# Kernel tuning notes

Measured on AMD Instinct MI355X. Metric: run time of the kernel, lower is better.

The kernel has to match this reference:

```python
import jax, jax.numpy as jnp
import numpy as np

HEADS = 16
HEAD_DIM = 64
TOKEN_DIM = 1024
INNER = HEADS * HEAD_DIM


def setup_inputs() -> dict:
    key = jax.random.key(0)
    k1, k2, k3, k4 = jax.random.split(key, 4)
    x = jax.random.normal(k1, (2, 2048, TOKEN_DIM), dtype=jnp.float32)
    # nn.Linear(token_dim, inner*3, bias=False): weight [3*inner, token_dim]
    w_qkv = jax.random.normal(k2, (3 * INNER, TOKEN_DIM), dtype=jnp.float32) * (TOKEN_DIM ** -0.5)
    # nn.Linear(inner, token_dim): weight [token_dim, inner], bias [token_dim]
    w_out = jax.random.normal(k3, (TOKEN_DIM, INNER), dtype=jnp.float32) * (INNER ** -0.5)
    b_out = jax.random.normal(k4, (TOKEN_DIM,), dtype=jnp.float32) * 0.01
    return {"x": x, "w_qkv": w_qkv, "w_out": w_out, "b_out": b_out}


def reference(x, w_qkv, w_out, b_out):
    b, n, _ = x.shape
    scale = HEAD_DIM ** -0.5
    qkv = x @ w_qkv.T                                  # [b, n, 3*inner]
    q, k, v = jnp.split(qkv, 3, axis=-1)
    def split_heads(t):
        return t.reshape(b, n, HEADS, HEAD_DIM).transpose(0, 2, 1, 3)  # [b,h,n,d]
    q, k, v = split_heads(q), split_heads(k), split_heads(v)
    dot = jnp.einsum('bhtd,bhsd->bhts', q, k) * scale  # [b,h,n,n]
    attn = jax.nn.softmax(dot, axis=-1)
    out = jnp.einsum('bhts,bhsd->bhtd', attn, v)       # [b,h,n,d]
    out = out.transpose(0, 2, 1, 3).reshape(b, n, INNER)
    return out @ w_out.T + b_out
```

## Files before the change

### kernel.cpp

```cpp
#include <hip/hip_runtime.h>
#include <hip/hip_bf16.h>

typedef short short4v __attribute__((ext_vector_type(4)));
typedef short short8 __attribute__((ext_vector_type(8)));
typedef float float4v __attribute__((ext_vector_type(4)));

#define HEADS 16
#define HDIM 64
#define TOKDIM 1024
#define SEQ 2048
#define BATCH 2
#define BH (BATCH*HEADS)
#define MROWS (BATCH*SEQ)

__device__ __forceinline__ short f2b(float f) {
    __hip_bfloat16 h = __float2bfloat16(f);
    return *reinterpret_cast<short*>(&h);
}
__device__ __forceinline__ float b2f(short s) {
    __hip_bfloat16 h;
    *reinterpret_cast<short*>(&h) = s;
    return __bfloat162float(h);
}
__device__ __forceinline__ short8 load8_f32_bf16(const float* __restrict__ p) {
    float4v a = *(const float4v*)p;
    float4v b = *(const float4v*)(p + 4);
    short8 r;
    r[0]=f2b(a[0]); r[1]=f2b(a[1]); r[2]=f2b(a[2]); r[3]=f2b(a[3]);
    r[4]=f2b(b[0]); r[5]=f2b(b[1]); r[6]=f2b(b[2]); r[7]=f2b(b[3]);
    return r;
}
__device__ __forceinline__ int packrn(float a, float b) {
    unsigned ua = __float_as_uint(a) + 0x8000u;
    unsigned ub = __float_as_uint(b) + 0x8000u;
    return (int)__builtin_amdgcn_perm(ub, ua, 0x07060302u);
}
__device__ __forceinline__ float hexp2(float x) {
    return __builtin_amdgcn_exp2f(x);
}

__device__ __forceinline__ void stage16(const void* g, void* l) {
    __builtin_amdgcn_global_load_lds((const __attribute__((address_space(1))) void*)g,
                                     (__attribute__((address_space(3))) void*)l, 16, 0, 0);
}

__global__ __launch_bounds__(256)
void cvt_bf16(const float* __restrict__ x,  short* __restrict__ xb,  int n8x,
              const float* __restrict__ wq, short* __restrict__ wqb, int n8q,
              const float* __restrict__ wo, short* __restrict__ wob, int n8o)
{
    int i = blockIdx.x*256 + threadIdx.x;
    const float* s; short* d; int off;
    if (i < n8x)                  { s = x;  d = xb;  off = i; }
    else if (i < n8x + n8q)       { s = wq; d = wqb; off = i - n8x; }
    else if (i < n8x + n8q + n8o) { s = wo; d = wob; off = i - n8x - n8q; }
    else return;
    *(short8*)&d[(size_t)off*8] = load8_f32_bf16(&s[(size_t)off*8]);
}

template<int ABF16>
__global__ __launch_bounds__(256)
void gemm_qkv(const void* __restrict__ Ap, const short* __restrict__ Wq,
              short* __restrict__ Qo, short* __restrict__ Ko, short* __restrict__ Vto)
{
    __shared__ __align__(16) short As[128*32];
    __shared__ __align__(16) short Bs[128*32];
    const int tid  = threadIdx.x;
    const int lane = tid & 63;
    const int wave = tid >> 6;
    const int wm = wave >> 1, wn = wave & 1;
    const int m0 = blockIdx.x * 128;
    const int n0 = blockIdx.y * 128;
    const int col16 = lane & 15, quad = lane >> 4;

    const int srow = lane >> 2;
    const int scol = (lane & 3) * 8;

    float4v acc[4][4];
    #pragma unroll
    for (int i=0;i<4;i++)
        #pragma unroll
        for (int j=0;j<4;j++) acc[i][j] = (float4v){0.f,0.f,0.f,0.f};

    for (int k0 = 0; k0 < TOKDIM; k0 += 32) {
        __syncthreads();
        if (ABF16) {
            const short* A = (const short*)Ap;
            #pragma unroll
            for (int j=0;j<2;++j) {
                const int rb = (wave*2 + j) * 16;
                stage16(&A[(size_t)(m0 + rb + srow)*TOKDIM + k0 + scol], &As[rb*32]);
            }
        } else {
            const float* A = (const float*)Ap;
            #pragma unroll
            for (int s=0;s<2;++s) {
                int blk = tid + s*256;
                int r = blk >> 2, kb = blk & 3;
                *(short8*)&As[r*32 + kb*8] = load8_f32_bf16(&A[(size_t)(m0+r)*TOKDIM + k0 + kb*8]);
            }
        }
        #pragma unroll
        for (int j=0;j<2;++j) {
            const int rb = (wave*2 + j) * 16;
            stage16(&Wq[(size_t)(n0 + rb + srow)*TOKDIM + k0 + scol], &Bs[rb*32]);
        }
        __syncthreads();

        short8 af[4], bfr[4];
        #pragma unroll
        for (int i=0;i<4;i++) af[i]  = *(const short8*)&As[(wm*64 + i*16 + col16)*32 + quad*8];
        #pragma unroll
        for (int j=0;j<4;j++) bfr[j] = *(const short8*)&Bs[(wn*64 + j*16 + col16)*32 + quad*8];
        #pragma unroll
        for (int i=0;i<4;i++)
            #pragma unroll
            for (int j=0;j<4;j++)
                acc[i][j] = __builtin_amdgcn_mfma_f32_16x16x32_bf16(af[i], bfr[j], acc[i][j], 0,0,0);
    }

    #pragma unroll
    for (int i=0;i<4;i++)
        #pragma unroll
        for (int j=0;j<4;j++) {
            const int n = n0 + wn*64 + j*16 + col16;
            const int part = n >> 10;
            const int h = (n & 1023) >> 6;
            const int d = n & 63;
            const int mb = m0 + wm*64 + i*16 + quad*4;
            const int b = mb >> 11;
            const int t = mb & 2047;
            if (part == 2) {
                union { short4v s; int2 i2; } w;
                #pragma unroll
                for (int r=0;r<4;r++) w.s[r] = f2b(acc[i][j][r]);
                *(int2*)&Vto[((size_t)(b*HEADS + h)*HDIM + d)*SEQ + t] = w.i2;
            } else {
                short* dst = (part == 0) ? Qo : Ko;
                #pragma unroll
                for (int r=0;r<4;r++)
                    dst[((size_t)(b*HEADS + h)*SEQ + t + r)*HDIM + d] = f2b(acc[i][j][r]);
            }
        }
}

#define OBM 64
#define OBN 128
#define OBK 64
#define OKT (TOKDIM/OBK)

__global__ __launch_bounds__(256)
void gemm_out(const short* __restrict__ A, const short* __restrict__ W,
              const float* __restrict__ bias, float* __restrict__ C)
{
    __shared__ __align__(16) short Asl[2*OBM*OBK];
    __shared__ __align__(16) short Bsl[2*OBN*OBK];
    const int tid  = threadIdx.x;
    const int lane = tid & 63;
    const int wave = tid >> 6;
    const int wm = wave >> 1, wn = wave & 1;
    const int m0 = blockIdx.x * OBM;
    const int n0 = blockIdx.y * OBN;
    const int col16 = lane & 15, quad = lane >> 4;

    const int srow = lane >> 3;
    const int scol = (((lane & 7) ^ srow) << 3);

    const int r7 = col16 & 7;
    const int rdoff0 = ((0*4 + quad) ^ r7) << 3;
    const int rdoff1 = ((1*4 + quad) ^ r7) << 3;

    float4v acc[2][4];
    #pragma unroll
    for (int i=0;i<2;i++)
        #pragma unroll
        for (int j=0;j<4;j++) acc[i][j] = (float4v){0.f,0.f,0.f,0.f};

    #pragma unroll
    for (int c=0;c<2;++c) {
        const int rb = (wave*2 + c)*8;
        stage16(&A[(size_t)(m0 + rb + srow)*TOKDIM + scol], &Asl[rb*OBK]);
    }
    #pragma unroll
    for (int c=0;c<4;++c) {
        const int rb = (wave*4 + c)*8;
        stage16(&W[(size_t)(n0 + rb + srow)*TOKDIM + scol], &Bsl[rb*OBK]);
    }
    asm volatile("s_waitcnt vmcnt(0)" ::: "memory");
    __builtin_amdgcn_s_barrier();

    for (int kt = 0; kt < OKT; ++kt) {
        const int buf = kt & 1;
        const short* Ab = &Asl[buf*OBM*OBK];
        const short* Bb = &Bsl[buf*OBN*OBK];
        short* An = &Asl[(buf^1)*OBM*OBK];
        short* Bn = &Bsl[(buf^1)*OBN*OBK];

        if (kt + 1 < OKT) {
            const int k1 = (kt + 1)*OBK;
            #pragma unroll
            for (int c=0;c<2;++c) {
                const int rb = (wave*2 + c)*8;
                stage16(&A[(size_t)(m0 + rb + srow)*TOKDIM + k1 + scol], &An[rb*OBK]);
            }
            #pragma unroll
            for (int c=0;c<4;++c) {
                const int rb = (wave*4 + c)*8;
                stage16(&W[(size_t)(n0 + rb + srow)*TOKDIM + k1 + scol], &Bn[rb*OBK]);
            }
        }

        #pragma unroll
        for (int kk=0;kk<2;++kk) {
            const int rdoff = kk ? rdoff1 : rdoff0;
            short8 af[2], bfr[4];
            #pragma unroll
            for (int i=0;i<2;i++)
                af[i]  = *(const short8*)&Ab[(wm*32 + i*16 + col16)*OBK + rdoff];
            #pragma unroll
            for (int j=0;j<4;j++)
                bfr[j] = *(const short8*)&Bb[(wn*64 + j*16 + col16)*OBK + rdoff];
            __builtin_amdgcn_s_setprio(1);
            #pragma unroll
            for (int i=0;i<2;i++)
                #pragma unroll
                for (int j=0;j<4;j++)
                    acc[i][j] = __builtin_amdgcn_mfma_f32_16x16x32_bf16(af[i], bfr[j], acc[i][j], 0,0,0);
            __builtin_amdgcn_s_setprio(0);
        }

        asm volatile("s_waitcnt vmcnt(0)" ::: "memory");
        __builtin_amdgcn_s_barrier();
    }

    #pragma unroll
    for (int i=0;i<2;i++)
        #pragma unroll
        for (int j=0;j<4;j++) {
            const int n = n0 + wn*64 + j*16 + col16;
            const float bn = bias[n];
            #pragma unroll
            for (int r=0;r<4;r++) {
                const int m = m0 + wm*32 + i*16 + quad*4 + r;
                C[(size_t)m*TOKDIM + n] = acc[i][j][r] + bn;
            }
        }
}

#define AQB 128
#define KT  64
#define NTH 16
#define KVT (KT*HDIM)
#define BUF2 (2*KVT)

__global__ __launch_bounds__(256, 2)
void attn_kernel(const short* __restrict__ Q, const short* __restrict__ K,
                 const short* __restrict__ Vt, short* __restrict__ AO)
{
    __shared__ __align__(16) short SL[2*2*BUF2];

    const int tid   = threadIdx.x;
    const int lane  = tid & 63;
    const int wave  = tid >> 6;
    const int col16 = lane & 15, quad = lane >> 4;
    const int bh  = blockIdx.y;
    const int qh  = wave & 1;
    const int kh2 = wave >> 1;
    const int qb  = blockIdx.x*AQB + qh*64;

    const short* Qb = Q  + (size_t)bh*SEQ*HDIM;
    const short* Kb = K  + (size_t)bh*SEQ*HDIM;
    const short* Vb = Vt + (size_t)bh*HDIM*SEQ;

    short* Sbase = &SL[kh2*2*BUF2];
    const int kbase = kh2 * 1024;

    const int w   = wave & 1;
    const int l3  = lane >> 3;
    const int scsw = (((lane & 7) ^ l3) << 4) >> 1;
    int krow[4], vrow[4];
    #pragma unroll
    for (int c=0;c<4;++c) {
        const int s = w*32 + c*8 + l3;
        krow[c] = (s&32) + ((s&12)<<1) + ((s&16)>>2) + (s&3);
        vrow[c] = s;
    }

    const int r7 = col16 & 7;
    int scol2[2];
    #pragma unroll
    for (int j=0;j<2;++j)
        scol2[j] = ((((j<<6) | (quad<<4)) ^ (r7<<4)) >> 1);

    const float qscale = 0.125f * 1.44269504088896f;
    short8 qf[4][2];
    #pragma unroll
    for (int qg=0; qg<4; ++qg)
        #pragma unroll
        for (int kk=0; kk<2; ++kk) {
            short8 raw = *(const short8*)&Qb[(size_t)(qb+qg*16+col16)*HDIM + kk*32 + quad*8];
            #pragma unroll
            for (int j=0;j<8;++j) raw[j] = f2b(b2f(raw[j]) * qscale);
            qf[qg][kk] = raw;
        }

    const short one_bf16 = (short)0x3F80;
    const short8 vones = {one_bf16, one_bf16, one_bf16, one_bf16,
                          one_bf16, one_bf16, one_bf16, one_bf16};

    float4v o[4][4];
    float4v o1[4];
    #pragma unroll
    for (int qg=0;qg<4;qg++) {
        #pragma unroll
        for (int dt=0;dt<4;dt++) o[qg][dt] = (float4v){0.f,0.f,0.f,0.f};
        o1[qg] = (float4v){0.f,0.f,0.f,0.f};
    }

    {
        short* Kn = Sbase;
        short* Vn = Sbase + KVT;
        #pragma unroll
        for (int c=0;c<4;++c) {
            stage16(&Kb[(size_t)(kbase + krow[c])*HDIM + scsw], &Kn[w*2048 + c*512]);
            stage16(&Vb[(size_t)vrow[c]*SEQ + kbase + scsw],    &Vn[w*2048 + c*512]);
        }
    }
    __syncthreads();

    for (int t = 0; t < NTH; ++t) {
        short* Kc = Sbase + (t & 1)*BUF2;
        short* Vc = Kc + KVT;

        if (t + 1 < NTH) {
            const int g1 = kbase + (t+1)*KT;
            short* Kn = Sbase + ((t & 1)^1)*BUF2;
            short* Vn = Kn + KVT;
            #pragma unroll
            for (int c=0;c<4;++c) {
                stage16(&Kb[(size_t)(g1 + krow[c])*HDIM + scsw], &Kn[w*2048 + c*512]);
                stage16(&Vb[(size_t)vrow[c]*SEQ + g1 + scsw],    &Vn[w*2048 + c*512]);
            }
        }

        #pragma unroll
        for (int kk = 0; kk < 2; ++kk) {
            short8 ka[2][2];
            #pragma unroll
            for (int nt=0; nt<2; ++nt)
                #pragma unroll
                for (int kh=0; kh<2; ++kh)
                    ka[nt][kh] = *(const short8*)&Kc[(kk*32 + nt*16 + col16)*64 + scol2[kh]];
            short8 va[4];
            #pragma unroll
            for (int dt=0; dt<4; ++dt)
                va[dt] = *(const short8*)&Vc[(dt*16 + col16)*64 + scol2[kk]];

            #pragma unroll
            for (int qg=0; qg<4; ++qg) {
                float4v st[2];
                __builtin_amdgcn_s_setprio(1);
                #pragma unroll
                for (int nt=0; nt<2; ++nt) {
                    float4v z = (float4v){0.f,0.f,0.f,0.f};
                    z = __builtin_amdgcn_mfma_f32_16x16x32_bf16(ka[nt][0], qf[qg][0], z, 0,0,0);
                    z = __builtin_amdgcn_mfma_f32_16x16x32_bf16(ka[nt][1], qf[qg][1], z, 0,0,0);
                    st[nt] = z;
                }
                __builtin_amdgcn_s_setprio(0);
                union { int i[4]; short8 s8; } pb;
                float p00 = hexp2(st[0][0]), p01 = hexp2(st[0][1]);
                float p02 = hexp2(st[0][2]), p03 = hexp2(st[0][3]);
                float p10 = hexp2(st[1][0]), p11 = hexp2(st[1][1]);
                float p12 = hexp2(st[1][2]), p13 = hexp2(st[1][3]);
                pb.i[0] = packrn(p00, p01); pb.i[1] = packrn(p02, p03);
                pb.i[2] = packrn(p10, p11); pb.i[3] = packrn(p12, p13);

                __builtin_amdgcn_s_setprio(1);
                #pragma unroll
                for (int dt=0; dt<4; ++dt)
                    o[qg][dt] = __builtin_amdgcn_mfma_f32_16x16x32_bf16(va[dt], pb.s8, o[qg][dt], 0,0,0);
                o1[qg] = __builtin_amdgcn_mfma_f32_16x16x32_bf16(vones, pb.s8, o1[qg], 0,0,0);
                __builtin_amdgcn_s_setprio(0);
            }
        }

        __syncthreads();
    }

    float lsum[4];
    #pragma unroll
    for (int qg=0; qg<4; ++qg) lsum[qg] = o1[qg][0];

    float* M = (float*)SL;
    float* Mw = M + (qh*64 + lane)*68;
    if (kh2 == 1) {
        #pragma unroll
        for (int qg=0; qg<4; ++qg) {
            #pragma unroll
            for (int dt=0; dt<4; ++dt)
                *(float4v*)&Mw[(qg*4+dt)*4] = o[qg][dt];
            Mw[64+qg] = lsum[qg];
        }
    }
    __syncthreads();
    if (kh2 == 0) {
        const int b = bh >> 4, h = bh & 15;
        #pragma unroll
        for (int qg=0; qg<4; ++qg) {
            lsum[qg] += Mw[64+qg];
            const float inv = 1.0f / lsum[qg];
            const int tq = qb + qg*16 + col16;
            #pragma unroll
            for (int dt=0; dt<4; ++dt) {
                float4v ov = o[qg][dt] + *(const float4v*)&Mw[(qg*4+dt)*4];
                union { short4v s; int2 i2; } w2;
                #pragma unroll
                for (int r=0;r<4;++r) w2.s[r] = f2b(ov[r] * inv);
                *(int2*)&AO[((size_t)(b*SEQ + tq))*TOKDIM + h*64 + dt*16 + quad*4] = w2.i2;
            }
        }
    }
}

extern "C" void kernel_launch(void* const* d_in, const int* in_sizes, int n_in,
                              void* d_out, int out_size, void* d_ws, size_t ws_size,
                              hipStream_t stream)
{
    const float* x    = (const float*)d_in[0];
    const float* wqkv = (const float*)d_in[1];
    const float* wout = (const float*)d_in[2];
    const float* bout = (const float*)d_in[3];
    float* out = (float*)d_out;

    char* ws = (char*)d_ws;
    const size_t SZ   = (size_t)BH*SEQ*HDIM*sizeof(short);
    const size_t WQB  = (size_t)3*TOKDIM*TOKDIM*sizeof(short);
    const size_t WOB  = (size_t)TOKDIM*TOKDIM*sizeof(short);
    const size_t NEED_FULL = SZ + WQB + WOB + 3*SZ;
    const bool full = ws_size >= NEED_FULL;

    short *Xb, *Wqb, *Wob, *Qt, *Kt, *Vt, *AO;
    if (full) {
        Xb  = (short*)ws;
        Wqb = (short*)(ws + SZ);
        Wob = (short*)(ws + SZ + WQB);
        Qt  = (short*)(ws + SZ + WQB + WOB);
        Kt  = Qt + SZ/2;
        Vt  = Kt + SZ/2;
        AO  = Xb;
    } else {
        Xb  = nullptr;
        Wqb = (short*)ws;
        Wob = (short*)(ws + WQB);
        Qt  = (short*)(ws + WQB + WOB);
        Kt  = Qt + SZ/2;
        Vt  = Kt + SZ/2;
        AO  = Vt + SZ/2;
    }

    const int n8x = full ? (BATCH*SEQ*TOKDIM)/8 : 0;
    const int n8q = (3*TOKDIM*TOKDIM)/8;
    const int n8o = (TOKDIM*TOKDIM)/8;
    const int cvt_blocks = (n8x + n8q + n8o + 255) / 256;
    cvt_bf16<<<cvt_blocks, 256, 0, stream>>>(x, Xb, n8x, wqkv, Wqb, n8q, wout, Wob, n8o);

    if (full)
        gemm_qkv<1><<<dim3(MROWS/128, (3*TOKDIM)/128), 256, 0, stream>>>(
            (const void*)Xb, Wqb, Qt, Kt, Vt);
    else
        gemm_qkv<0><<<dim3(MROWS/128, (3*TOKDIM)/128), 256, 0, stream>>>(
            (const void*)x, Wqb, Qt, Kt, Vt);

    attn_kernel<<<dim3(SEQ/AQB, BH), 256, 0, stream>>>(Qt, Kt, Vt, AO);

    gemm_out<<<dim3(MROWS/OBM, TOKDIM/OBN), 256, 0, stream>>>(AO, Wob, bout, out);
}
```

Baseline: 170.1 us.

## Double-buffer LDS tiles in QKV GEMM to overlap global loads with MFMA

Doubles the shared-memory tiles in the QKV projection GEMM and prefetches the next K-slice into the alternate buffer while the current slice feeds the MFMAs. This leaves a single barrier per iteration instead of two, and raises wave priority around the MFMA block with s_setprio. The cost is twice the LDS per block, which may reduce occupancy. The explicit vmcnt(0) wait at the end of each iteration still blocks on the prefetch, so the overlap is limited to one iteration's compute.

```diff
diff --git a/kernel.cpp b/kernel.cpp
--- a/kernel.cpp
+++ b/kernel.cpp
@@ -63,8 +63,8 @@
 void gemm_qkv(const void* __restrict__ Ap, const short* __restrict__ Wq,
               short* __restrict__ Qo, short* __restrict__ Ko, short* __restrict__ Vto)
 {
-    __shared__ __align__(16) short As[128*32];
-    __shared__ __align__(16) short Bs[128*32];
+    __shared__ __align__(16) short As[2*128*32];
+    __shared__ __align__(16) short Bs[2*128*32];
     const int tid  = threadIdx.x;
     const int lane = tid & 63;
     const int wave = tid >> 6;
@@ -82,41 +82,77 @@
         #pragma unroll
         for (int j=0;j<4;j++) acc[i][j] = (float4v){0.f,0.f,0.f,0.f};
 
-    for (int k0 = 0; k0 < TOKDIM; k0 += 32) {
-        __syncthreads();
-        if (ABF16) {
-            const short* A = (const short*)Ap;
+    if (ABF16) {
+        const short* A = (const short*)Ap;
+        #pragma unroll
+        for (int j=0;j<2;++j) {
+            const int rb = (wave*2 + j) * 16;
+            stage16(&A[(size_t)(m0 + rb + srow)*TOKDIM + scol], &As[rb*32]);
+        }
+    } else {
+        const float* A = (const float*)Ap;
+        #pragma unroll
+        for (int s=0;s<2;++s) {
+            int blk = tid + s*256;
+            int r = blk >> 2, kb = blk & 3;
+            *(short8*)&As[r*32 + kb*8] = load8_f32_bf16(&A[(size_t)(m0+r)*TOKDIM + kb*8]);
+        }
+    }
+    #pragma unroll
+    for (int j=0;j<2;++j) {
+        const int rb = (wave*2 + j) * 16;
+        stage16(&Wq[(size_t)(n0 + rb + srow)*TOKDIM + scol], &Bs[rb*32]);
+    }
+    asm volatile("s_waitcnt vmcnt(0) lgkmcnt(0)" ::: "memory");
+    __builtin_amdgcn_s_barrier();
+
+    for (int kt = 0; kt < 32; ++kt) {
+        const int buf = kt & 1;
+        const short* Ab = &As[buf*4096];
+        const short* Bb = &Bs[buf*4096];
+        short* An = &As[(buf^1)*4096];
+        short* Bn = &Bs[(buf^1)*4096];
+
+        if (kt + 1 < 32) {
+            const int k1 = (kt + 1) * 32;
+            if (ABF16) {
+                const short* A = (const short*)Ap;
+                #pragma unroll
+                for (int j=0;j<2;++j) {
+                    const int rb = (wave*2 + j) * 16;
+                    stage16(&A[(size_t)(m0 + rb + srow)*TOKDIM + k1 + scol], &An[rb*32]);
+                }
+            } else {
+                const float* A = (const float*)Ap;
+                #pragma unroll
+                for (int s=0;s<2;++s) {
+                    int blk = tid + s*256;
+                    int r = blk >> 2, kb = blk & 3;
+                    *(short8*)&An[r*32 + kb*8] = load8_f32_bf16(&A[(size_t)(m0+r)*TOKDIM + k1 + kb*8]);
+                }
+            }
             #pragma unroll
             for (int j=0;j<2;++j) {
                 const int rb = (wave*2 + j) * 16;
-                stage16(&A[(size_t)(m0 + rb + srow)*TOKDIM + k0 + scol], &As[rb*32]);
-            }
-        } else {
-            const float* A = (const float*)Ap;
-            #pragma unroll
-            for (int s=0;s<2;++s) {
-                int blk = tid + s*256;
-                int r = blk >> 2, kb = blk & 3;
-                *(short8*)&As[r*32 + kb*8] = load8_f32_bf16(&A[(size_t)(m0+r)*TOKDIM + k0 + kb*8]);
-            }
-        }
-        #pragma unroll
-        for (int j=0;j<2;++j) {
-            const int rb = (wave*2 + j) * 16;
-            stage16(&Wq[(size_t)(n0 + rb + srow)*TOKDIM + k0 + scol], &Bs[rb*32]);
-        }
-        __syncthreads();
+                stage16(&Wq[(size_t)(n0 + rb + srow)*TOKDIM + k1 + scol], &Bn[rb*32]);
+            }
+        }
 
         short8 af[4], bfr[4];
         #pragma unroll
-        for (int i=0;i<4;i++) af[i]  = *(const short8*)&As[(wm*64 + i*16 + col16)*32 + quad*8];
-        #pragma unroll
-        for (int j=0;j<4;j++) bfr[j] = *(const short8*)&Bs[(wn*64 + j*16 + col16)*32 + quad*8];
+        for (int i=0;i<4;i++) af[i]  = *(const short8*)&Ab[(wm*64 + i*16 + col16)*32 + quad*8];
+        #pragma unroll
+        for (int j=0;j<4;j++) bfr[j] = *(const short8*)&Bb[(wn*64 + j*16 + col16)*32 + quad*8];
+        __builtin_amdgcn_s_setprio(1);
         #pragma unroll
         for (int i=0;i<4;i++)
             #pragma unroll
             for (int j=0;j<4;j++)
                 acc[i][j] = __builtin_amdgcn_mfma_f32_16x16x32_bf16(af[i], bfr[j], acc[i][j], 0,0,0);
+        __builtin_amdgcn_s_setprio(0);
+
+        asm volatile("s_waitcnt vmcnt(0) lgkmcnt(0)" ::: "memory");
+        __builtin_amdgcn_s_barrier();
     }
 
     #pragma unroll
```

Result: slower. 174.0 us (+2.3%).
